# Performance work log

Measured on AMD Instinct MI355X. Metric: run time of the kernel, lower is better.

The kernel has to match this reference:

```python
import jax, jax.numpy as jnp
import numpy as np
from jax import lax

ALPHA = 0.2  # tf.nn.leaky_relu default
EPS = 1e-3   # keras BatchNormalization default epsilon


def _conv(x, w):
    return lax.conv_general_dilated(x, w, (1, 1), 'SAME',
                                    dimension_numbers=('NHWC', 'HWIO', 'NHWC'))


def _bn(x, g, b, m, v):
    return (x - m) * (g * lax.rsqrt(v + EPS)) + b


def _subpixel(x):
    B, H, W, C = x.shape
    G = C // 4
    x = x.reshape(B, H, W, G, 2, 2)          # (n,y,x,g,hi,wi)
    x = x.transpose(0, 1, 5, 2, 4, 3)        # (n,y,wi,x,hi,g)
    return x.reshape(B, 2 * H, 2 * W, G)


def _leaky(x):
    return jnp.where(x >= 0, x, ALPHA * x)


def setup_inputs() -> dict:
    key = jax.random.key(0)
    ks = jax.random.split(key, 4)
    B, H, W, C = 16, 128, 128, 64
    F = 64
    d = {
        'x':  jax.random.normal(ks[0], (B, H, W, C), jnp.float32),
        'W1': jax.random.normal(ks[1], (3, 3, C, 4 * F), jnp.float32) * 0.05,
        'b1': jnp.zeros((4 * F,), jnp.float32),
        'g1': jnp.ones((4 * F,), jnp.float32),
        'be1': jnp.zeros((4 * F,), jnp.float32),
        'm1': jnp.zeros((4 * F,), jnp.float32),
        'v1': jnp.ones((4 * F,), jnp.float32),
        'W2': jax.random.normal(ks[2], (3, 3, F, F), jnp.float32) * 0.05,
        'b2': jnp.zeros((F,), jnp.float32),
        'g2': jnp.ones((F,), jnp.float32),
        'be2': jnp.zeros((F,), jnp.float32),
        'm2': jnp.zeros((F,), jnp.float32),
        'v2': jnp.ones((F,), jnp.float32),
        'Wu': jax.random.normal(ks[3], (1, 1, C, F), jnp.float32) * 0.05,
        'bu': jnp.zeros((F,), jnp.float32),
    }
    return d


def reference(x, W1, b1, g1, be1, m1, v1, W2, b2, g2, be2, m2, v2, Wu, bu):
    out = _leaky(_bn(_conv(x, W1) + b1, g1, be1, m1, v1))
    out = _subpixel(out)                                   # (B,2H,2W,F)
    out = _leaky(_bn(_conv(out, W2) + b2, g2, be2, m2, v2))
    idn = jnp.repeat(jnp.repeat(x, 2, axis=1), 2, axis=2)
    idn = _conv(idn, Wu) + bu
    return _leaky(out + idn)
```

## Files before the change

kernel.cpp:

```cpp
#include <hip/hip_runtime.h>
#include <hip/hip_bf16.h>

#define ALPHA 0.2f
#define EPS 1e-3f

typedef __bf16 bf16x8 __attribute__((ext_vector_type(8)));
typedef float f32x4 __attribute__((ext_vector_type(4)));

constexpr int B_  = 16;
constexpr int H_  = 128, W_ = 128;
constexpr int HP  = 130, WP = 130;
constexpr int H2  = 256, W2 = 256;
constexpr int H2P = 258, W2P = 258;

constexpr size_t OFF_XPAD = 0;
constexpr size_t OFF_T1   = 34611200;
constexpr size_t OFF_PW1  = OFF_T1 + 136323072;
constexpr size_t OFF_PW2  = OFF_PW1 + 294912;
constexpr size_t OFF_SC   = OFF_PW2 + 81920;

__device__ __forceinline__ void gload_lds16(const void* g, void* l) {
    __builtin_amdgcn_global_load_lds(
        (const __attribute__((address_space(1))) unsigned int*)g,
        (__attribute__((address_space(3))) unsigned int*)l, 16, 0, 0);
}


__global__ void prep_scales(const float* b1, const float* g1, const float* be1,
                            const float* m1, const float* v1,
                            const float* b2, const float* g2, const float* be2,
                            const float* m2, const float* v2,
                            float* sc) {
    int t = threadIdx.x;
    if (t < 256) {
        float s = g1[t] * rsqrtf(v1[t] + EPS);
        sc[t]       = s;
        sc[256 + t] = (b1[t] - m1[t]) * s + be1[t];
    }
    if (t < 64) {
        float s = g2[t] * rsqrtf(v2[t] + EPS);
        sc[512 + t] = s;
        sc[576 + t] = (b2[t] - m2[t]) * s + be2[t];
    }
}

__global__ void pack_w(const float* W1f, const float* W2f, const float* Wuf,
                       __hip_bfloat16* pw1, __hip_bfloat16* pw2) {
    int blk = blockIdx.x;
    int l = threadIdx.x;
    if (blk < 288) {
        int kt = blk / 16, nt = blk % 16;
        #pragma unroll
        for (int j = 0; j < 8; ++j) {
            int k = kt * 32 + (l >> 4) * 8 + j;
            int n = nt * 16 + (l & 15);
            pw1[blk * 512 + l * 8 + j] = __float2bfloat16(W1f[k * 256 + n]);
        }
    } else {
        int bi = blk - 288;
        int kt = bi / 4, nt = bi % 4;
        #pragma unroll
        for (int j = 0; j < 8; ++j) {
            int k = kt * 32 + (l >> 4) * 8 + j;
            int n = nt * 16 + (l & 15);
            float v = (k < 576) ? W2f[k * 64 + n] : Wuf[(k - 576) * 64 + n];
            pw2[bi * 512 + l * 8 + j] = __float2bfloat16(v);
        }
    }
}

__global__ void pad_x(const float* x, __hip_bfloat16* xp, int total8) {
    for (int e = blockIdx.x * blockDim.x + threadIdx.x; e < total8;
         e += gridDim.x * blockDim.x) {
        int c8 = (e & 7) * 8;
        int t = e >> 3;
        int xx = t % WP; t /= WP;
        int yy = t % HP; t /= HP;
        int n = t;
        union { bf16x8 v; __hip_bfloat16 h[8]; } o;
        if (yy >= 1 && yy <= H_ && xx >= 1 && xx <= W_) {
            const float* src = x + ((size_t)(n * H_ + (yy - 1)) * W_ + (xx - 1)) * 64 + c8;
            float4 f0 = *(const float4*)src;
            float4 f1 = *(const float4*)(src + 4);
            o.h[0] = __float2bfloat16(f0.x); o.h[1] = __float2bfloat16(f0.y);
            o.h[2] = __float2bfloat16(f0.z); o.h[3] = __float2bfloat16(f0.w);
            o.h[4] = __float2bfloat16(f1.x); o.h[5] = __float2bfloat16(f1.y);
            o.h[6] = __float2bfloat16(f1.z); o.h[7] = __float2bfloat16(f1.w);
        } else {
            #pragma unroll
            for (int j = 0; j < 8; ++j) o.h[j] = __float2bfloat16(0.f);
        }
        *(bf16x8*)(xp + (size_t)e * 8) = o.v;
    }
}

__global__ void zero_t1_border(__hip_bfloat16* t1) {
    int e = blockIdx.x * blockDim.x + threadIdx.x;
    if (e >= 16 * 1028 * 64) return;
    int c = e & 63;
    int t = e >> 6;
    int p = t % 1028;
    int n = t / 1028;
    int yy, xx;
    if (p < 258)      { yy = 0;   xx = p; }
    else if (p < 516) { yy = 257; xx = p - 258; }
    else { int p2 = p - 516; yy = 1 + (p2 >> 1); xx = (p2 & 1) ? 257 : 0; }
    t1[((n * H2P + yy) * W2P + xx) * 64 + c] = __float2bfloat16(0.f);
}

__global__ __launch_bounds__(256, 3)
void gemm1(const __hip_bfloat16* xp, const __hip_bfloat16* pw1,
           const float* sc, __hip_bfloat16* t1) {
    __shared__ __hip_bfloat16 lds_a[2][4608];
    __shared__ __hip_bfloat16 lds_t1[2 * 128 * 64];

    int bid = blockIdx.x;
    int b = (bid & 7) * 512 + (bid >> 3);
    int n = b >> 8;
    int y = (b >> 1) & 127;
    int x0 = (b & 1) * 64;
    int w = threadIdx.x >> 6;
    int l = threadIdx.x & 63;
    int lr = l & 15, lk = l >> 4;

    const __hip_bfloat16* Bbase = pw1 + (size_t)(w * 4) * 512 + l * 8;
    f32x4 acc[4][4] = {};
    bf16x8 abuf[2][4], bbuf[2][4];

    #define STAGE1(ky_, buf_) do {                                            \
        const char* rowg = (const char*)(xp +                                 \
            ((size_t)(n * HP + y + (ky_)) * WP + x0) * 64);                   \
        for (int j = w; j < 9; j += 4) {                                      \
            int off = j * 1024 + l * 16;                                      \
            int p = off >> 7, s2 = (off >> 4) & 7;                            \
            gload_lds16(rowg + (size_t)p * 128 + ((s2 ^ (p & 7)) << 4),       \
                        (char*)lds_a[buf_] + j * 1024);                       \
        } } while (0)

    #define ALOAD1(dst, buf_, j_) do {                                        \
        int kx = (j_) >> 1;                                                   \
        int o = ((j_) & 1) * 64 + lk * 16;                                    \
        _Pragma("unroll")                                                     \
        for (int mi = 0; mi < 4; ++mi) {                                      \
            int p = mi * 16 + lr + kx;                                        \
            abuf[dst][mi] = *(const bf16x8*)((const char*)lds_a[buf_] +       \
                p * 128 + (o ^ ((p & 7) << 4)));                              \
        } } while (0)

    #define BLOAD1(s_, kt_) do {                                              \
        const __hip_bfloat16* bp = Bbase + (size_t)(kt_) * 16 * 512;          \
        _Pragma("unroll")                                                     \
        for (int ni = 0; ni < 4; ++ni)                                        \
            bbuf[s_][ni] = *(const bf16x8*)(bp + ni * 512);                   \
        } while (0)

    STAGE1(0, 0);
    BLOAD1(0, 0);
    BLOAD1(1, 1);
    __syncthreads();

    #pragma unroll
    for (int ky = 0; ky < 3; ++ky) {
        if (ky < 2) STAGE1(ky + 1, (ky + 1) & 1);
        ALOAD1(0, ky & 1, 0);
        #pragma unroll
        for (int j = 0; j < 6; ++j) {
            int kt = ky * 6 + j;
            if (j < 5) ALOAD1((j + 1) & 1, ky & 1, j + 1);
            #pragma unroll
            for (int mi = 0; mi < 4; ++mi)
                #pragma unroll
                for (int ni = 0; ni < 4; ++ni)
                    acc[mi][ni] = __builtin_amdgcn_mfma_f32_16x16x32_bf16(
                        abuf[j & 1][mi], bbuf[kt & 1][ni], acc[mi][ni], 0, 0, 0);
            if (kt + 2 < 18) BLOAD1(kt & 1, kt + 2);
        }
        if (ky < 2) __syncthreads();
    }
    #undef STAGE1
    #undef ALOAD1
    #undef BLOAD1

    #pragma unroll
    for (int ni = 0; ni < 4; ++ni) {
        int c = w * 64 + ni * 16 + lr;
        float s  = sc[c];
        float sh = sc[256 + c];
        int g  = c >> 2;
        int hi = (c >> 1) & 1;
        int wi = c & 1;
        #pragma unroll
        for (int mi = 0; mi < 4; ++mi) {
            #pragma unroll
            for (int r = 0; r < 4; ++r) {
                int xl = mi * 16 + lk * 4 + r;
                float v = acc[mi][ni][r] * s + sh;
                v = (v >= 0.f) ? v : ALPHA * v;
                lds_t1[(wi * 128 + 2 * xl + hi) * 64 + g] = __float2bfloat16(v);
            }
        }
    }
    __syncthreads();
    #pragma unroll
    for (int wi_ = 0; wi_ < 2; ++wi_) {
        char* dst = (char*)(t1 + ((size_t)(n * H2P + 2 * y + wi_ + 1) * W2P
                                  + 2 * x0 + 1) * 64);
        const char* src = (const char*)lds_t1 + wi_ * 16384;
        #pragma unroll
        for (int it = 0; it < 4; ++it) {
            int off = it * 4096 + threadIdx.x * 16;
            *(float4*)(dst + off) = *(const float4*)(src + off);
        }
    }
}

__global__ __launch_bounds__(256, 3)
void gemm2(const __hip_bfloat16* t1, const __hip_bfloat16* xp,
           const __hip_bfloat16* pw2, const float* sc, const float* bu,
           float* out) {
    __shared__ alignas(16) char smem[2 * 17408 + 8448];
    __hip_bfloat16* lds_idn = (__hip_bfloat16*)(smem + 2 * 17408);

    int bid = blockIdx.x;
    int b = (bid & 7) * 1024 + (bid >> 3);
    int n = b >> 9;
    int Y = (b >> 1) & 255;
    int X0 = (b & 1) * 128;
    int w = threadIdx.x >> 6;
    int l = threadIdx.x & 63;
    int lr = l & 15, lk = l >> 4;
    int wpx = w & 1;
    int wni = w >> 1;

    bf16x8 abuf[2][4], bbuf[2][2];

    #define STAGE2(ky_, buf_) do {                                            \
        const char* rowg = (const char*)t1 +                                  \
            ((size_t)(n * H2P + Y + (ky_)) * W2P + X0) * 128;                 \
        for (int j = w; j < 17; j += 4) {                                     \
            int off = j * 1024 + l * 16;                                      \
            int p = off >> 7, s2 = (off >> 4) & 7;                            \
            gload_lds16(rowg + (size_t)p * 128 + ((s2 ^ (p & 7)) << 4),       \
                        smem + (buf_) * 17408 + j * 1024);                    \
        } } while (0)

    #define ALOAD2(dst, buf_, j_) do {                                        \
        int kx = (j_) >> 1;                                                   \
        int o = ((j_) & 1) * 64 + lk * 16;                                    \
        _Pragma("unroll")                                                     \
        for (int mi = 0; mi < 4; ++mi) {                                      \
            int p = wpx * 64 + mi * 16 + lr + kx;                             \
            abuf[dst][mi] = *(const bf16x8*)(smem + (buf_) * 17408 +          \
                p * 128 + (o ^ ((p & 7) << 4)));                              \
        } } while (0)

    #define BLOAD2(s_, kt_) do {                                              \
        const __hip_bfloat16* bp = pw2 +                                      \
            ((size_t)(kt_) * 4 + wni * 2) * 512 + l * 8;                      \
        _Pragma("unroll")                                                     \
        for (int ni = 0; ni < 2; ++ni)                                        \
            bbuf[s_][ni] = *(const bf16x8*)(bp + ni * 512);                   \
        } while (0)

    bf16x8 pa[2], pb[2][4];
    #pragma unroll
    for (int kt2 = 0; kt2 < 2; ++kt2) {
        int ci0 = kt2 * 32 + lk * 8;
        int u = (X0 >> 1) + w * 16 + lr;
        pa[kt2] = *(const bf16x8*)(
            xp + ((size_t)(n * HP + (Y >> 1) + 1) * WP + u + 1) * 64 + ci0);
        const __hip_bfloat16* bp = pw2 + (size_t)((18 + kt2) * 4) * 512 + l * 8;
        #pragma unroll
        for (int ni = 0; ni < 4; ++ni)
            pb[kt2][ni] = *(const bf16x8*)(bp + ni * 512);
    }
    STAGE2(0, 0);
    BLOAD2(0, 0);
    BLOAD2(1, 1);

    {
        f32x4 aid[4] = {};
        #pragma unroll
        for (int kt2 = 0; kt2 < 2; ++kt2)
            #pragma unroll
            for (int ni = 0; ni < 4; ++ni)
                aid[ni] = __builtin_amdgcn_mfma_f32_16x16x32_bf16(
                    pa[kt2], pb[kt2][ni], aid[ni], 0, 0, 0);
        #pragma unroll
        for (int ni = 0; ni < 4; ++ni) {
            int c = ni * 16 + lr;
            float bc = bu[c];
            #pragma unroll
            for (int r = 0; r < 4; ++r) {
                int u = w * 16 + lk * 4 + r;
                lds_idn[u * 66 + c] = __float2bfloat16(aid[ni][r] + bc);
            }
        }
    }
    __syncthreads();

    f32x4 am[4][2] = {};
    #pragma unroll
    for (int ky = 0; ky < 3; ++ky) {
        if (ky < 2) STAGE2(ky + 1, (ky + 1) & 1);
        ALOAD2(0, ky & 1, 0);
        #pragma unroll
        for (int j = 0; j < 6; ++j) {
            int kt = ky * 6 + j;
            if (j < 5) ALOAD2((j + 1) & 1, ky & 1, j + 1);
            #pragma unroll
            for (int mi = 0; mi < 4; ++mi)
                #pragma unroll
                for (int ni = 0; ni < 2; ++ni)
                    am[mi][ni] = __builtin_amdgcn_mfma_f32_16x16x32_bf16(
                        abuf[j & 1][mi], bbuf[kt & 1][ni], am[mi][ni], 0, 0, 0);
            if (kt + 2 < 18) BLOAD2(kt & 1, kt + 2);
        }
        if (ky < 2) __syncthreads();
    }
    #undef STAGE2
    #undef ALOAD2
    #undef BLOAD2

    __syncthreads();
    float* tr = (float*)smem;
    #pragma unroll
    for (int ni = 0; ni < 2; ++ni) {
        int c = wni * 32 + ni * 16 + lr;
        float s  = sc[512 + c];
        float sh = sc[576 + c];
        #pragma unroll
        for (int mi = 0; mi < 4; ++mi) {
            #pragma unroll
            for (int r = 0; r < 4; ++r) {
                int xl = wpx * 64 + mi * 16 + lk * 4 + r;
                float v = am[mi][ni][r] * s + sh;
                v = (v >= 0.f) ? v : ALPHA * v;
                v = v + __bfloat162float(lds_idn[(xl >> 1) * 66 + c]);
                v = (v >= 0.f) ? v : ALPHA * v;
                tr[xl * 68 + c] = v;
            }
        }
    }
    __syncthreads();
    float* orow = out + ((size_t)(n * H2 + Y) * W2 + X0) * 64;
    #pragma unroll
    for (int it = 0; it < 8; ++it) {
        int idx = it * 256 + threadIdx.x;
        int px = idx >> 4, cq = idx & 15;
        f32x4 v4 = *(const f32x4*)(tr + px * 68 + cq * 4);
        *(f32x4*)(orow + px * 64 + cq * 4) = v4;
    }
}


extern "C" void kernel_launch(void* const* d_in, const int* in_sizes, int n_in,
                              void* d_out, int out_size, void* d_ws, size_t ws_size,
                              hipStream_t stream) {
    const float* x   = (const float*)d_in[0];
    const float* W1  = (const float*)d_in[1];
    const float* b1  = (const float*)d_in[2];
    const float* g1  = (const float*)d_in[3];
    const float* be1 = (const float*)d_in[4];
    const float* m1  = (const float*)d_in[5];
    const float* v1  = (const float*)d_in[6];
    const float* W2  = (const float*)d_in[7];
    const float* b2  = (const float*)d_in[8];
    const float* g2  = (const float*)d_in[9];
    const float* be2 = (const float*)d_in[10];
    const float* m2  = (const float*)d_in[11];
    const float* v2  = (const float*)d_in[12];
    const float* Wu  = (const float*)d_in[13];
    const float* bu  = (const float*)d_in[14];
    float* out = (float*)d_out;

    char* ws = (char*)d_ws;
    __hip_bfloat16* xp  = (__hip_bfloat16*)(ws + OFF_XPAD);
    __hip_bfloat16* t1  = (__hip_bfloat16*)(ws + OFF_T1);
    __hip_bfloat16* pw1 = (__hip_bfloat16*)(ws + OFF_PW1);
    __hip_bfloat16* pw2 = (__hip_bfloat16*)(ws + OFF_PW2);
    float* sc = (float*)(ws + OFF_SC);

    prep_scales<<<1, 256, 0, stream>>>(b1, g1, be1, m1, v1, b2, g2, be2, m2, v2, sc);
    pack_w<<<368, 64, 0, stream>>>(W1, W2, Wu, pw1, pw2);
    pad_x<<<2048, 256, 0, stream>>>(x, xp, B_ * HP * WP * 8);
    zero_t1_border<<<(16 * 1028 * 64 + 255) / 256, 256, 0, stream>>>(t1);
    gemm1<<<4096, 256, 0, stream>>>(xp, pw1, sc, t1);
    gemm2<<<8192, 256, 0, stream>>>(t1, xp, pw2, sc, bu, out);
}
```

Before: 261.7 us.

## Retile gemm2 to two output rows by 64 pixels with all input rows staged

The second conv kernel now gives each block two output rows of 64 pixels instead of one row of 128. The four padded input rows those two rows need are loaded into shared memory once at the start. This lets the two rows share their halo rows, cutting global reads of t1, and removes the per-ky barriers in the main loop. Shared memory shrinks, so launch bounds rise to 4 blocks per CU, and the identity-branch 1x1 conv is computed once by two waves for both rows. Risks: the epilogue's transpose buffer uses a 66-float row stride, so some 16-byte shared-memory reads and writes are not 16-byte aligned, and two waves sit idle during the identity step.

```diff
diff --git a/kernel.cpp b/kernel.cpp
--- a/kernel.cpp
+++ b/kernel.cpp
@@ -214,71 +214,76 @@
     }
 }
 
-__global__ __launch_bounds__(256, 3)
+__global__ __launch_bounds__(256, 4)
 void gemm2(const __hip_bfloat16* t1, const __hip_bfloat16* xp,
            const __hip_bfloat16* pw2, const float* sc, const float* bu,
            float* out) {
-    __shared__ alignas(16) char smem[2 * 17408 + 8448];
-    __hip_bfloat16* lds_idn = (__hip_bfloat16*)(smem + 2 * 17408);
+    __shared__ alignas(16) char smem[4 * 8448 + 4224];
+    __hip_bfloat16* lds_idn = (__hip_bfloat16*)(smem + 4 * 8448);
 
     int bid = blockIdx.x;
     int b = (bid & 7) * 1024 + (bid >> 3);
     int n = b >> 9;
-    int Y = (b >> 1) & 255;
-    int X0 = (b & 1) * 128;
+    int rem = b & 511;
+    int Y0 = (rem >> 2) * 2;
+    int X0 = (rem & 3) * 64;
     int w = threadIdx.x >> 6;
     int l = threadIdx.x & 63;
     int lr = l & 15, lk = l >> 4;
-    int wpx = w & 1;
-    int wni = w >> 1;
+    int ry = w >> 1;
+    int nh = w & 1;
 
     bf16x8 abuf[2][4], bbuf[2][2];
 
-    #define STAGE2(ky_, buf_) do {                                            \
+    #define STAGE2(r_) do {                                                   \
         const char* rowg = (const char*)t1 +                                  \
-            ((size_t)(n * H2P + Y + (ky_)) * W2P + X0) * 128;                 \
-        for (int j = w; j < 17; j += 4) {                                     \
-            int off = j * 1024 + l * 16;                                      \
-            int p = off >> 7, s2 = (off >> 4) & 7;                            \
-            gload_lds16(rowg + (size_t)p * 128 + ((s2 ^ (p & 7)) << 4),       \
-                        smem + (buf_) * 17408 + j * 1024);                    \
+            ((size_t)(n * H2P + Y0 + (r_)) * W2P + X0) * 128;                 \
+        for (int j = w; j < 9; j += 4) {                                      \
+            if (j < 8 || l < 16) {                                            \
+                int off = j * 1024 + l * 16;                                  \
+                int p = off >> 7, s2 = (off >> 4) & 7;                        \
+                gload_lds16(rowg + (size_t)p * 128 + ((s2 ^ (p & 7)) << 4),   \
+                            smem + (r_) * 8448 + j * 1024);                   \
+            }                                                                 \
         } } while (0)
 
-    #define ALOAD2(dst, buf_, j_) do {                                        \
+    #define ALOAD2(dst, rb_, j_) do {                                         \
         int kx = (j_) >> 1;                                                   \
         int o = ((j_) & 1) * 64 + lk * 16;                                    \
         _Pragma("unroll")                                                     \
         for (int mi = 0; mi < 4; ++mi) {                                      \
-            int p = wpx * 64 + mi * 16 + lr + kx;                             \
-            abuf[dst][mi] = *(const bf16x8*)(smem + (buf_) * 17408 +          \
+            int p = mi * 16 + lr + kx;                                        \
+            abuf[dst][mi] = *(const bf16x8*)(smem + (rb_) * 8448 +            \
                 p * 128 + (o ^ ((p & 7) << 4)));                              \
         } } while (0)
 
     #define BLOAD2(s_, kt_) do {                                              \
         const __hip_bfloat16* bp = pw2 +                                      \
-            ((size_t)(kt_) * 4 + wni * 2) * 512 + l * 8;                      \
+            ((size_t)(kt_) * 4 + nh * 2) * 512 + l * 8;                       \
         _Pragma("unroll")                                                     \
         for (int ni = 0; ni < 2; ++ni)                                        \
             bbuf[s_][ni] = *(const bf16x8*)(bp + ni * 512);                   \
         } while (0)
 
     bf16x8 pa[2], pb[2][4];
-    #pragma unroll
-    for (int kt2 = 0; kt2 < 2; ++kt2) {
-        int ci0 = kt2 * 32 + lk * 8;
-        int u = (X0 >> 1) + w * 16 + lr;
-        pa[kt2] = *(const bf16x8*)(
-            xp + ((size_t)(n * HP + (Y >> 1) + 1) * WP + u + 1) * 64 + ci0);
-        const __hip_bfloat16* bp = pw2 + (size_t)((18 + kt2) * 4) * 512 + l * 8;
-        #pragma unroll
-        for (int ni = 0; ni < 4; ++ni)
-            pb[kt2][ni] = *(const bf16x8*)(bp + ni * 512);
-    }
-    STAGE2(0, 0);
+    if (w < 2) {
+        #pragma unroll
+        for (int kt2 = 0; kt2 < 2; ++kt2) {
+            int ci0 = kt2 * 32 + lk * 8;
+            int u = (X0 >> 1) + w * 16 + lr;
+            pa[kt2] = *(const bf16x8*)(
+                xp + ((size_t)(n * HP + (Y0 >> 1) + 1) * WP + u + 1) * 64 + ci0);
+            const __hip_bfloat16* bp = pw2 + (size_t)((18 + kt2) * 4) * 512 + l * 8;
+            #pragma unroll
+            for (int ni = 0; ni < 4; ++ni)
+                pb[kt2][ni] = *(const bf16x8*)(bp + ni * 512);
+        }
+    }
+    STAGE2(0); STAGE2(1); STAGE2(2); STAGE2(3);
     BLOAD2(0, 0);
     BLOAD2(1, 1);
 
-    {
+    if (w < 2) {
         f32x4 aid[4] = {};
         #pragma unroll
         for (int kt2 = 0; kt2 < 2; ++kt2)
@@ -302,12 +307,12 @@
     f32x4 am[4][2] = {};
     #pragma unroll
     for (int ky = 0; ky < 3; ++ky) {
-        if (ky < 2) STAGE2(ky + 1, (ky + 1) & 1);
-        ALOAD2(0, ky & 1, 0);
+        int rb = ry + ky;
+        ALOAD2(0, rb, 0);
         #pragma unroll
         for (int j = 0; j < 6; ++j) {
             int kt = ky * 6 + j;
-            if (j < 5) ALOAD2((j + 1) & 1, ky & 1, j + 1);
+            if (j < 5) ALOAD2((j + 1) & 1, rb, j + 1);
             #pragma unroll
             for (int mi = 0; mi < 4; ++mi)
                 #pragma unroll
@@ -316,7 +321,6 @@
                         abuf[j & 1][mi], bbuf[kt & 1][ni], am[mi][ni], 0, 0, 0);
             if (kt + 2 < 18) BLOAD2(kt & 1, kt + 2);
         }
-        if (ky < 2) __syncthreads();
     }
     #undef STAGE2
     #undef ALOAD2
@@ -326,29 +330,31 @@
     float* tr = (float*)smem;
     #pragma unroll
     for (int ni = 0; ni < 2; ++ni) {
-        int c = wni * 32 + ni * 16 + lr;
+        int c = nh * 32 + ni * 16 + lr;
         float s  = sc[512 + c];
         float sh = sc[576 + c];
         #pragma unroll
         for (int mi = 0; mi < 4; ++mi) {
             #pragma unroll
             for (int r = 0; r < 4; ++r) {
-                int xl = wpx * 64 + mi * 16 + lk * 4 + r;
+                int xl = mi * 16 + lk * 4 + r;
                 float v = am[mi][ni][r] * s + sh;
                 v = (v >= 0.f) ? v : ALPHA * v;
                 v = v + __bfloat162float(lds_idn[(xl >> 1) * 66 + c]);
                 v = (v >= 0.f) ? v : ALPHA * v;
-                tr[xl * 68 + c] = v;
+                tr[(ry * 64 + xl) * 66 + c] = v;
             }
         }
     }
     __syncthreads();
-    float* orow = out + ((size_t)(n * H2 + Y) * W2 + X0) * 64;
     #pragma unroll
     for (int it = 0; it < 8; ++it) {
         int idx = it * 256 + threadIdx.x;
-        int px = idx >> 4, cq = idx & 15;
-        f32x4 v4 = *(const f32x4*)(tr + px * 68 + cq * 4);
+        int rr = idx >> 10;
+        int i = idx & 1023;
+        int px = i >> 4, cq = i & 15;
+        f32x4 v4 = *(const f32x4*)(tr + (rr * 64 + px) * 66 + cq * 4);
+        float* orow = out + ((size_t)(n * H2 + Y0 + rr) * W2 + X0) * 64;
         *(f32x4*)(orow + px * 64 + cq * 4) = v4;
     }
 }
```

Result: no change. 257.7 us (-1.5%).
